# Performance work log

Measured on AMD Instinct MI355X. Metric: run time of the kernel, lower is better.

Reference implementation:

```python
import jax, jax.numpy as jnp
import numpy as np

B, H, I = 4096, 128, 128


def setup_inputs() -> dict:
    key = jax.random.key(0)
    ks = jax.random.split(key, 9)
    # xavier_uniform for W1/W2: fan_in = 2H*2I, fan_out = H*2I (torch treats dim0 as fan_out for >2D differently,
    # but we only need a plausible init; exact init values don't affect correctness of the math)
    def xavier(k, shape):
        fan_in = shape[1] * shape[2] if len(shape) == 3 else shape[0]
        fan_out = shape[0] * shape[2] if len(shape) == 3 else shape[1]
        lim = np.sqrt(6.0 / (fan_in + fan_out))
        return jax.random.uniform(k, shape, jnp.float32, -lim, lim)
    W1 = xavier(ks[0], (H, 2 * H, 2 * I))
    W2 = xavier(ks[1], (H, 2 * H, 2 * I))
    W3 = xavier(ks[2], (2 * H, H))
    fan_in, fan_out = 2 * H * 2 * I, H * 2 * I
    lim = float(np.sqrt(3.0 / (0.5 * (fan_in + fan_out))))
    b1 = jax.random.uniform(ks[3], (H,), jnp.float32, -lim, lim)
    b2 = jax.random.uniform(ks[4], (H,), jnp.float32, -lim, lim)
    in0 = jax.random.normal(ks[5], (B, I), jnp.float32)
    in1 = jax.random.normal(ks[6], (B, I), jnp.float32)
    st0 = jax.random.normal(ks[7], (B, H), jnp.float32)
    st1 = jax.random.normal(ks[8], (B, H), jnp.float32)
    return {"in0": in0, "in1": in1, "st0": st0, "st1": st1,
            "W1": W1, "b1": b1, "W2": W2, "b2": b2, "W3": W3}


def reference(in0, in1, st0, st1, W1, b1, W2, b2, W3):
    s = jnp.concatenate([st0, st1], axis=1)  # [B, 2H]
    x = jnp.concatenate([in0, in1], axis=1)  # [B, 2I]
    # Trilinear contraction; same math as outer-product-then-contract:
    # einsum('ij,ik->ijk') then ('ijk,ljk->il')  ==  'bj,bk,ljk->bl'
    m1 = jnp.einsum('bj,bk,ljk->bl', s, x, W1)  # [B, H]
    m2 = jnp.einsum('bj,bk,ljk->bl', s, x, W2)  # [B, H]
    u = jax.nn.sigmoid(m2 + b2)
    state_tilda = jnp.tanh(m1 + b1)
    new_state = u * state_tilda + (1.0 - u) * (s @ W3)
    return new_state
```

## Files before the change

kernel.cpp:

```cpp
#include <hip/hip_runtime.h>
#include <hip/hip_bf16.h>
#include <stdint.h>


typedef short bf8 __attribute__((ext_vector_type(8)));
typedef float f32x4 __attribute__((ext_vector_type(4)));

static constexpr size_t WT_OFF  = 0;
static constexpr size_t XBF_OFF = 33554432 + 2097152;
static constexpr size_t MP_OFF  = XBF_OFF + 2097152;

__device__ __forceinline__ unsigned f2bf(float f) {
    unsigned u = __builtin_bit_cast(unsigned, f);
    return (u + 0x7fffu + ((u >> 16) & 1u)) >> 16;
}
__device__ __forceinline__ unsigned pack2bf(float a, float b) {
    return f2bf(a) | (f2bf(b) << 16);
}

__global__ void prep_wx(const float* __restrict__ W1, const float* __restrict__ W2,
                        const float* __restrict__ in0, const float* __restrict__ in1,
                        uint4* __restrict__ Wt, unsigned* __restrict__ x_bf) {
    int bx = blockIdx.x;
    if (bx < 8192) {
        const int tid  = threadIdx.x;
        const int lane = tid & 63, wave = tid >> 6;
        const unsigned f = bx * 4 + wave;
        const unsigned n16 = f >> 11;
        const unsigned kchunk = (f >> 1) & 1023u;
        const unsigned kst = f & 1u;
        const unsigned n = n16 * 16 + (lane & 15);
        const unsigned K = kchunk * 64 + kst * 32 + (lane >> 4) * 8;
        const float* src = (n < 128 ? W1 + ((size_t)n << 16)
                                    : W2 + ((size_t)(n - 128) << 16)) + K;
        float4 a = ((const float4*)src)[0];
        float4 b = ((const float4*)src)[1];
        uint4 o;
        o.x = pack2bf(a.x, a.y); o.y = pack2bf(a.z, a.w);
        o.z = pack2bf(b.x, b.y); o.w = pack2bf(b.z, b.w);
        Wt[(size_t)f * 64 + lane] = o;
    } else {
        unsigned v = (bx - 8192) * 256 + threadIdx.x;
        unsigned b = v >> 6;
        unsigned j4 = (v & 63u) * 4u;
        const float* src = (j4 < 128) ? (in0 + (size_t)b * 128 + j4)
                                      : (in1 + (size_t)b * 128 + (j4 - 128));
        float4 a = *(const float4*)src;
        uint2 o;
        o.x = pack2bf(a.x, a.y);
        o.y = pack2bf(a.z, a.w);
        ((uint2*)x_bf)[v] = o;
    }
}

__launch_bounds__(256, 2)
__global__ void gemm_p(const unsigned char* __restrict__ Wt,
                       const float* __restrict__ st0, const float* __restrict__ st1,
                       const __hip_bfloat16* __restrict__ x_bf,
                       float* __restrict__ Mpart) {
    const int bx = blockIdx.x;
    const int ks = bx & 7;
    const int nt = (bx >> 3) & 1;
    const int mt = bx >> 4;
    const int b0 = mt << 7, n0 = nt << 7;
    const int tid  = threadIdx.x;
    const int lane = tid & 63, wave = tid >> 6;
    const int l15 = lane & 15, l4 = lane >> 4;

    __shared__ __align__(16) float Sl[32 * 132];
    for (int idx = tid; idx < 4096; idx += 256) {
        int r = idx >> 5, j = idx & 31;
        int jg = ks * 32 + j;
        float v = (jg < 128) ? st0[(size_t)(b0 + r) * 128 + jg]
                             : st1[(size_t)(b0 + r) * 128 + (jg - 128)];
        Sl[j * 132 + r] = v;
    }
    __syncthreads();

    const int n16_0 = __builtin_amdgcn_readfirstlane(nt * 8 + wave * 2 + 0);
    const int n16_1 = __builtin_amdgcn_readfirstlane(nt * 8 + wave * 2 + 1);
    const unsigned char* wb0 = Wt + ((size_t)n16_0 << 21);
    const unsigned char* wb1 = Wt + ((size_t)n16_1 << 21);

    f32x4 racc[8][2];
    #pragma unroll
    for (int mf = 0; mf < 8; ++mf)
        #pragma unroll
        for (int nf = 0; nf < 2; ++nf)
            racc[mf][nf] = (f32x4){0.f, 0.f, 0.f, 0.f};
    const f32x4 zacc = (f32x4){0.f, 0.f, 0.f, 0.f};

    bf8 a[8][2];
    bf8 buf[2][2][2];

    unsigned vo = (unsigned)lane * 16u + (unsigned)ks * 262144u;

    for (int q = 0; q < 4; ++q) {
        #pragma unroll
        for (int mf = 0; mf < 8; ++mf) {
            const __hip_bfloat16* xp =
                x_bf + (size_t)((b0 + mf * 16 + l15) * 256 + q * 64 + l4 * 8);
            a[mf][0] = *(const bf8*)(xp);
            a[mf][1] = *(const bf8*)(xp + 32);
        }
        buf[0][0][0] = *(const bf8*)(wb0 + vo);
        buf[0][0][1] = *(const bf8*)(wb0 + vo + 1024);
        buf[0][1][0] = *(const bf8*)(wb1 + vo);
        buf[0][1][1] = *(const bf8*)(wb1 + vo + 1024);
        vo += 8192;

        const float* svp = Sl + l4 * 4;

        for (int jb = 0; jb < 4; ++jb) {
            #pragma unroll
            for (int jj = 0; jj < 8; ++jj) {
                const int pp = jj & 1;
                buf[pp ^ 1][0][0] = *(const bf8*)(wb0 + vo);
                buf[pp ^ 1][0][1] = *(const bf8*)(wb0 + vo + 1024);
                buf[pp ^ 1][1][0] = *(const bf8*)(wb1 + vo);
                buf[pp ^ 1][1][1] = *(const bf8*)(wb1 + vo + 1024);
                vo += 8192;
                f32x4 sv[8];
                #pragma unroll
                for (int mf = 0; mf < 8; ++mf)
                    sv[mf] = *(const f32x4*)(svp + mf * 16);
                svp += 132;
                #pragma unroll
                for (int nf = 0; nf < 2; ++nf) {
                    bf8 bf0 = buf[pp][nf][0];
                    bf8 bf1 = buf[pp][nf][1];
                    #pragma unroll
                    for (int mf = 0; mf < 8; ++mf) {
                        f32x4 m0 = __builtin_amdgcn_mfma_f32_16x16x32_bf16(a[mf][0], bf0, zacc, 0, 0, 0);
                        m0 = __builtin_amdgcn_mfma_f32_16x16x32_bf16(a[mf][1], bf1, m0, 0, 0, 0);
                        racc[mf][nf] += sv[mf] * m0;
                    }
                }
            }
        }
        vo += 2048 - 33 * 8192;
    }

    float* mp = Mpart + ((size_t)ks << 20);
    #pragma unroll
    for (int mf = 0; mf < 8; ++mf)
        #pragma unroll
        for (int nf = 0; nf < 2; ++nf) {
            int b = b0 + mf * 16 + l4 * 4;
            int n = n0 + wave * 32 + nf * 16 + l15;
            #pragma unroll
            for (int r = 0; r < 4; ++r)
                mp[(size_t)(b + r) * 256 + n] = racc[mf][nf][r];
        }
}

__global__ void epilogue(const float* __restrict__ st0, const float* __restrict__ st1,
                         const float* __restrict__ b1, const float* __restrict__ b2,
                         const float* __restrict__ W3, const float* __restrict__ Mpart,
                         float* __restrict__ out) {
    const int tid = threadIdx.x;
    const int h = tid & 127, rg = tid >> 7;
    const int bbase = blockIdx.x * 8;
    __shared__ float srow[8][256];
    #pragma unroll
    for (int i = 0; i < 8; ++i) {
        int idx = i * 256 + tid;
        int r = idx >> 8, j = idx & 255;
        float v = (j < 128) ? st0[(size_t)(bbase + r) * 128 + j]
                            : st1[(size_t)(bbase + r) * 128 + (j - 128)];
        srow[r][j] = v;
    }
    __syncthreads();
    float acc0 = 0.f, acc1 = 0.f, acc2 = 0.f, acc3 = 0.f;
    for (int j = 0; j < 256; ++j) {
        float w = W3[j * 128 + h];
        acc0 += srow[rg][j] * w;
        acc1 += srow[rg + 2][j] * w;
        acc2 += srow[rg + 4][j] * w;
        acc3 += srow[rg + 6][j] * w;
    }
    float accs[4] = {acc0, acc1, acc2, acc3};
    float bb1 = b1[h], bb2 = b2[h];
    #pragma unroll
    for (int i = 0; i < 4; ++i) {
        int b = bbase + rg + i * 2;
        float m1 = 0.f, m2 = 0.f;
        #pragma unroll
        for (int k = 0; k < 8; ++k) {
            m1 += Mpart[((size_t)k << 20) + (size_t)b * 256 + h];
            m2 += Mpart[((size_t)k << 20) + (size_t)b * 256 + 128 + h];
        }
        float u = 1.0f / (1.0f + expf(-(m2 + bb2)));
        float t = tanhf(m1 + bb1);
        out[(size_t)b * 128 + h] = u * t + (1.0f - u) * accs[i];
    }
}

extern "C" void kernel_launch(void* const* d_in, const int* in_sizes, int n_in,
                              void* d_out, int out_size, void* d_ws, size_t ws_size,
                              hipStream_t stream) {
    const float* in0 = (const float*)d_in[0];
    const float* in1 = (const float*)d_in[1];
    const float* st0 = (const float*)d_in[2];
    const float* st1 = (const float*)d_in[3];
    const float* W1  = (const float*)d_in[4];
    const float* b1  = (const float*)d_in[5];
    const float* W2  = (const float*)d_in[6];
    const float* b2  = (const float*)d_in[7];
    const float* W3  = (const float*)d_in[8];
    float* out = (float*)d_out;
    char* ws = (char*)d_ws;

    unsigned char* Wt   = (unsigned char*)(ws + WT_OFF);
    unsigned*      x_bf = (unsigned*)(ws + XBF_OFF);
    float*         Mp   = (float*)(ws + MP_OFF);

    prep_wx<<<9216, 256, 0, stream>>>(W1, W2, in0, in1, (uint4*)Wt, x_bf);
    gemm_p<<<512, 256, 0, stream>>>(Wt, st0, st1, (const __hip_bfloat16*)x_bf, Mp);
    epilogue<<<512, 256, 0, stream>>>(st0, st1, b1, b2, W3, Mp, out);
}
```

Baseline: 251.8 us.

## Switch trilinear GEMM to 32x32x16 MFMA tiles with matching weight layout

The weight pre-pack layout is changed to 32-wide n fragments, and the main kernel now uses 32x32x16 bf16 MFMAs, with each wave owning one 32-column slice and four 32-row tiles. Four chained MFMAs cover a 64-wide k chunk before the per-row state scale is applied. The aim is higher MFMA throughput per instruction and fewer weight/x loads per FLOP. It keeps 64 accumulator floats per lane plus operand registers. Separately, the epilogue is split into twice as many blocks of 4 rows, with its inner loop unrolled, for more parallelism.

```diff
diff --git a/kernel.cpp b/kernel.cpp
--- a/kernel.cpp
+++ b/kernel.cpp
@@ -5,6 +5,7 @@
 
 typedef short bf8 __attribute__((ext_vector_type(8)));
 typedef float f32x4 __attribute__((ext_vector_type(4)));
+typedef float f32x16 __attribute__((ext_vector_type(16)));
 
 static constexpr size_t WT_OFF  = 0;
 static constexpr size_t XBF_OFF = 33554432 + 2097152;
@@ -26,11 +27,11 @@
         const int tid  = threadIdx.x;
         const int lane = tid & 63, wave = tid >> 6;
         const unsigned f = bx * 4 + wave;
-        const unsigned n16 = f >> 11;
-        const unsigned kchunk = (f >> 1) & 1023u;
-        const unsigned kst = f & 1u;
-        const unsigned n = n16 * 16 + (lane & 15);
-        const unsigned K = kchunk * 64 + kst * 32 + (lane >> 4) * 8;
+        const unsigned n32 = f >> 12;
+        const unsigned kchunk = (f >> 2) & 1023u;
+        const unsigned ksub = f & 3u;
+        const unsigned n = n32 * 32 + (lane & 31);
+        const unsigned K = kchunk * 64 + ksub * 16 + (lane >> 5) * 8;
         const float* src = (n < 128 ? W1 + ((size_t)n << 16)
                                     : W2 + ((size_t)(n - 128) << 16)) + K;
         float4 a = ((const float4*)src)[0];
@@ -65,7 +66,7 @@
     const int b0 = mt << 7, n0 = nt << 7;
     const int tid  = threadIdx.x;
     const int lane = tid & 63, wave = tid >> 6;
-    const int l15 = lane & 15, l4 = lane >> 4;
+    const int l31 = lane & 31, hi = lane >> 5;
 
     __shared__ __align__(16) float Sl[32 * 132];
     for (int idx = tid; idx < 4096; idx += 256) {
@@ -77,80 +78,75 @@
     }
     __syncthreads();
 
-    const int n16_0 = __builtin_amdgcn_readfirstlane(nt * 8 + wave * 2 + 0);
-    const int n16_1 = __builtin_amdgcn_readfirstlane(nt * 8 + wave * 2 + 1);
-    const unsigned char* wb0 = Wt + ((size_t)n16_0 << 21);
-    const unsigned char* wb1 = Wt + ((size_t)n16_1 << 21);
-
-    f32x4 racc[8][2];
-    #pragma unroll
-    for (int mf = 0; mf < 8; ++mf)
-        #pragma unroll
-        for (int nf = 0; nf < 2; ++nf)
-            racc[mf][nf] = (f32x4){0.f, 0.f, 0.f, 0.f};
-    const f32x4 zacc = (f32x4){0.f, 0.f, 0.f, 0.f};
-
-    bf8 a[8][2];
-    bf8 buf[2][2][2];
-
-    unsigned vo = (unsigned)lane * 16u + (unsigned)ks * 262144u;
+    const int n32 = __builtin_amdgcn_readfirstlane(nt * 4 + wave);
+    const unsigned char* wb = Wt + ((size_t)n32 << 22);
+
+    f32x16 racc[4];
+    #pragma unroll
+    for (int mf = 0; mf < 4; ++mf)
+        #pragma unroll
+        for (int e = 0; e < 16; ++e) racc[mf][e] = 0.f;
+    f32x16 z16;
+    #pragma unroll
+    for (int e = 0; e < 16; ++e) z16[e] = 0.f;
+
+    bf8 a[4][4];
+    bf8 buf[2][4];
+
+    unsigned vo = (unsigned)lane * 16u + (unsigned)ks * 524288u;
 
     for (int q = 0; q < 4; ++q) {
         #pragma unroll
-        for (int mf = 0; mf < 8; ++mf) {
+        for (int mf = 0; mf < 4; ++mf) {
             const __hip_bfloat16* xp =
-                x_bf + (size_t)((b0 + mf * 16 + l15) * 256 + q * 64 + l4 * 8);
-            a[mf][0] = *(const bf8*)(xp);
-            a[mf][1] = *(const bf8*)(xp + 32);
-        }
-        buf[0][0][0] = *(const bf8*)(wb0 + vo);
-        buf[0][0][1] = *(const bf8*)(wb0 + vo + 1024);
-        buf[0][1][0] = *(const bf8*)(wb1 + vo);
-        buf[0][1][1] = *(const bf8*)(wb1 + vo + 1024);
-        vo += 8192;
-
-        const float* svp = Sl + l4 * 4;
-
-        for (int jb = 0; jb < 4; ++jb) {
+                x_bf + (size_t)((b0 + mf * 32 + l31) * 256 + q * 64 + hi * 8);
             #pragma unroll
-            for (int jj = 0; jj < 8; ++jj) {
-                const int pp = jj & 1;
-                buf[pp ^ 1][0][0] = *(const bf8*)(wb0 + vo);
-                buf[pp ^ 1][0][1] = *(const bf8*)(wb0 + vo + 1024);
-                buf[pp ^ 1][1][0] = *(const bf8*)(wb1 + vo);
-                buf[pp ^ 1][1][1] = *(const bf8*)(wb1 + vo + 1024);
-                vo += 8192;
-                f32x4 sv[8];
+            for (int ksub = 0; ksub < 4; ++ksub)
+                a[mf][ksub] = *(const bf8*)(xp + ksub * 16);
+        }
+        #pragma unroll
+        for (int ksub = 0; ksub < 4; ++ksub)
+            buf[0][ksub] = *(const bf8*)(wb + vo + ksub * 1024);
+        vo += 16384;
+
+        const float* svp = Sl + hi * 4;
+
+        for (int jb = 0; jb < 16; ++jb) {
+            #pragma unroll
+            for (int jj = 0; jj < 2; ++jj) {
+                const int pp = jj;
                 #pragma unroll
-                for (int mf = 0; mf < 8; ++mf)
-                    sv[mf] = *(const f32x4*)(svp + mf * 16);
-                svp += 132;
+                for (int ksub = 0; ksub < 4; ++ksub)
+                    buf[pp ^ 1][ksub] = *(const bf8*)(wb + vo + ksub * 1024);
+                vo += 16384;
                 #pragma unroll
-                for (int nf = 0; nf < 2; ++nf) {
-                    bf8 bf0 = buf[pp][nf][0];
-                    bf8 bf1 = buf[pp][nf][1];
+                for (int mf = 0; mf < 4; ++mf) {
+                    f32x16 m0 = __builtin_amdgcn_mfma_f32_32x32x16_bf16(a[mf][0], buf[pp][0], z16, 0, 0, 0);
+                    m0 = __builtin_amdgcn_mfma_f32_32x32x16_bf16(a[mf][1], buf[pp][1], m0, 0, 0, 0);
+                    m0 = __builtin_amdgcn_mfma_f32_32x32x16_bf16(a[mf][2], buf[pp][2], m0, 0, 0, 0);
+                    m0 = __builtin_amdgcn_mfma_f32_32x32x16_bf16(a[mf][3], buf[pp][3], m0, 0, 0, 0);
                     #pragma unroll
-                    for (int mf = 0; mf < 8; ++mf) {
-                        f32x4 m0 = __builtin_amdgcn_mfma_f32_16x16x32_bf16(a[mf][0], bf0, zacc, 0, 0, 0);
-                        m0 = __builtin_amdgcn_mfma_f32_16x16x32_bf16(a[mf][1], bf1, m0, 0, 0, 0);
-                        racc[mf][nf] += sv[mf] * m0;
+                    for (int g = 0; g < 4; ++g) {
+                        f32x4 sg = *(const f32x4*)(svp + mf * 32 + g * 8);
+                        #pragma unroll
+                        for (int t = 0; t < 4; ++t)
+                            racc[mf][g * 4 + t] += sg[t] * m0[g * 4 + t];
                     }
                 }
+                svp += 132;
             }
         }
-        vo += 2048 - 33 * 8192;
+        vo += 4096 - 33 * 16384;
     }
 
     float* mp = Mpart + ((size_t)ks << 20);
-    #pragma unroll
-    for (int mf = 0; mf < 8; ++mf)
-        #pragma unroll
-        for (int nf = 0; nf < 2; ++nf) {
-            int b = b0 + mf * 16 + l4 * 4;
-            int n = n0 + wave * 32 + nf * 16 + l15;
-            #pragma unroll
-            for (int r = 0; r < 4; ++r)
-                mp[(size_t)(b + r) * 256 + n] = racc[mf][nf][r];
+    const int n = n0 + (n32 & 3) * 32 + l31;
+    #pragma unroll
+    for (int mf = 0; mf < 4; ++mf)
+        #pragma unroll
+        for (int r = 0; r < 16; ++r) {
+            int row = b0 + mf * 32 + (r & 3) + 8 * (r >> 2) + 4 * hi;
+            mp[(size_t)row * 256 + n] = racc[mf][r];
         }
 }
 
@@ -160,10 +156,10 @@
                          float* __restrict__ out) {
     const int tid = threadIdx.x;
     const int h = tid & 127, rg = tid >> 7;
-    const int bbase = blockIdx.x * 8;
-    __shared__ float srow[8][256];
-    #pragma unroll
-    for (int i = 0; i < 8; ++i) {
+    const int bbase = blockIdx.x * 4;
+    __shared__ float srow[4][256];
+    #pragma unroll
+    for (int i = 0; i < 4; ++i) {
         int idx = i * 256 + tid;
         int r = idx >> 8, j = idx & 255;
         float v = (j < 128) ? st0[(size_t)(bbase + r) * 128 + j]
@@ -171,18 +167,17 @@
         srow[r][j] = v;
     }
     __syncthreads();
-    float acc0 = 0.f, acc1 = 0.f, acc2 = 0.f, acc3 = 0.f;
+    float acc0 = 0.f, acc1 = 0.f;
+    #pragma unroll 8
     for (int j = 0; j < 256; ++j) {
         float w = W3[j * 128 + h];
         acc0 += srow[rg][j] * w;
         acc1 += srow[rg + 2][j] * w;
-        acc2 += srow[rg + 4][j] * w;
-        acc3 += srow[rg + 6][j] * w;
-    }
-    float accs[4] = {acc0, acc1, acc2, acc3};
+    }
+    float accs[2] = {acc0, acc1};
     float bb1 = b1[h], bb2 = b2[h];
     #pragma unroll
-    for (int i = 0; i < 4; ++i) {
+    for (int i = 0; i < 2; ++i) {
         int b = bbase + rg + i * 2;
         float m1 = 0.f, m2 = 0.f;
         #pragma unroll
@@ -217,5 +212,5 @@
 
     prep_wx<<<9216, 256, 0, stream>>>(W1, W2, in0, in1, (uint4*)Wt, x_bf);
     gemm_p<<<512, 256, 0, stream>>>(Wt, st0, st1, (const __hip_bfloat16*)x_bf, Mp);
-    epilogue<<<512, 256, 0, stream>>>(st0, st1, b1, b2, W3, Mp, out);
-}
+    epilogue<<<1024, 256, 0, stream>>>(st0, st1, b1, b2, W3, Mp, out);
+}
```

Measured after the change: 326.9 us. 29.8% more time.

## Reorder packed weight layout for sequential streaming, deepen prefetch, split epilogue finer

Applied to the files above, without the earlier changes.

The bf16 weight repack now orders fragments in the exact sequence each GEMM block consumes them (split, q, j, kst). Each wave then streams weights contiguously with a fixed 2 KB stride. The register prefetch ring grows from 2 to 4 stages, with three stages preloaded before the main loop, to hide more global-load latency. The epilogue handles 4 rows per block across 1024 blocks instead of 8 rows across 512, with an unrolled W3 loop, to raise parallelism. The deeper ring costs more VGPRs, which could strain the 2-blocks-per-CU launch bound.

```diff
diff --git a/kernel.cpp b/kernel.cpp
--- a/kernel.cpp
+++ b/kernel.cpp
@@ -27,8 +27,13 @@
         const int lane = tid & 63, wave = tid >> 6;
         const unsigned f = bx * 4 + wave;
         const unsigned n16 = f >> 11;
-        const unsigned kchunk = (f >> 1) & 1023u;
-        const unsigned kst = f & 1u;
+        const unsigned r2  = f & 2047u;
+        const unsigned ks  = r2 >> 8;
+        const unsigned rem = r2 & 255u;
+        const unsigned q   = rem >> 6;
+        const unsigned jl  = (rem >> 1) & 31u;
+        const unsigned kst = rem & 1u;
+        const unsigned kchunk = (ks * 32 + jl) * 4 + q;
         const unsigned n = n16 * 16 + (lane & 15);
         const unsigned K = kchunk * 64 + kst * 32 + (lane >> 4) * 8;
         const float* src = (n < 128 ? W1 + ((size_t)n << 16)
@@ -91,9 +96,18 @@
     const f32x4 zacc = (f32x4){0.f, 0.f, 0.f, 0.f};
 
     bf8 a[8][2];
-    bf8 buf[2][2][2];
+    bf8 buf[4][2][2];
 
     unsigned vo = (unsigned)lane * 16u + (unsigned)ks * 262144u;
+
+    #pragma unroll
+    for (int w = 0; w < 3; ++w) {
+        buf[w][0][0] = *(const bf8*)(wb0 + vo);
+        buf[w][0][1] = *(const bf8*)(wb0 + vo + 1024);
+        buf[w][1][0] = *(const bf8*)(wb1 + vo);
+        buf[w][1][1] = *(const bf8*)(wb1 + vo + 1024);
+        vo += 2048;
+    }
 
     for (int q = 0; q < 4; ++q) {
         #pragma unroll
@@ -103,23 +117,20 @@
             a[mf][0] = *(const bf8*)(xp);
             a[mf][1] = *(const bf8*)(xp + 32);
         }
-        buf[0][0][0] = *(const bf8*)(wb0 + vo);
-        buf[0][0][1] = *(const bf8*)(wb0 + vo + 1024);
-        buf[0][1][0] = *(const bf8*)(wb1 + vo);
-        buf[0][1][1] = *(const bf8*)(wb1 + vo + 1024);
-        vo += 8192;
 
         const float* svp = Sl + l4 * 4;
 
-        for (int jb = 0; jb < 4; ++jb) {
+        for (int jb = 0; jb < 8; ++jb) {
             #pragma unroll
-            for (int jj = 0; jj < 8; ++jj) {
-                const int pp = jj & 1;
-                buf[pp ^ 1][0][0] = *(const bf8*)(wb0 + vo);
-                buf[pp ^ 1][0][1] = *(const bf8*)(wb0 + vo + 1024);
-                buf[pp ^ 1][1][0] = *(const bf8*)(wb1 + vo);
-                buf[pp ^ 1][1][1] = *(const bf8*)(wb1 + vo + 1024);
-                vo += 8192;
+            for (int jj = 0; jj < 4; ++jj) {
+                {
+                    const int ps = (jj + 3) & 3;
+                    buf[ps][0][0] = *(const bf8*)(wb0 + vo);
+                    buf[ps][0][1] = *(const bf8*)(wb0 + vo + 1024);
+                    buf[ps][1][0] = *(const bf8*)(wb1 + vo);
+                    buf[ps][1][1] = *(const bf8*)(wb1 + vo + 1024);
+                    vo += 2048;
+                }
                 f32x4 sv[8];
                 #pragma unroll
                 for (int mf = 0; mf < 8; ++mf)
@@ -127,8 +138,8 @@
                 svp += 132;
                 #pragma unroll
                 for (int nf = 0; nf < 2; ++nf) {
-                    bf8 bf0 = buf[pp][nf][0];
-                    bf8 bf1 = buf[pp][nf][1];
+                    bf8 bf0 = buf[jj][nf][0];
+                    bf8 bf1 = buf[jj][nf][1];
                     #pragma unroll
                     for (int mf = 0; mf < 8; ++mf) {
                         f32x4 m0 = __builtin_amdgcn_mfma_f32_16x16x32_bf16(a[mf][0], bf0, zacc, 0, 0, 0);
@@ -138,7 +149,6 @@
                 }
             }
         }
-        vo += 2048 - 33 * 8192;
     }
 
     float* mp = Mpart + ((size_t)ks << 20);
@@ -160,10 +170,10 @@
                          float* __restrict__ out) {
     const int tid = threadIdx.x;
     const int h = tid & 127, rg = tid >> 7;
-    const int bbase = blockIdx.x * 8;
-    __shared__ float srow[8][256];
-    #pragma unroll
-    for (int i = 0; i < 8; ++i) {
+    const int bbase = blockIdx.x * 4;
+    __shared__ float srow[4][256];
+    #pragma unroll
+    for (int i = 0; i < 4; ++i) {
         int idx = i * 256 + tid;
         int r = idx >> 8, j = idx & 255;
         float v = (j < 128) ? st0[(size_t)(bbase + r) * 128 + j]
@@ -171,18 +181,17 @@
         srow[r][j] = v;
     }
     __syncthreads();
-    float acc0 = 0.f, acc1 = 0.f, acc2 = 0.f, acc3 = 0.f;
+    float acc0 = 0.f, acc1 = 0.f;
+    #pragma unroll 8
     for (int j = 0; j < 256; ++j) {
         float w = W3[j * 128 + h];
         acc0 += srow[rg][j] * w;
         acc1 += srow[rg + 2][j] * w;
-        acc2 += srow[rg + 4][j] * w;
-        acc3 += srow[rg + 6][j] * w;
-    }
-    float accs[4] = {acc0, acc1, acc2, acc3};
+    }
+    float accs[2] = {acc0, acc1};
     float bb1 = b1[h], bb2 = b2[h];
     #pragma unroll
-    for (int i = 0; i < 4; ++i) {
+    for (int i = 0; i < 2; ++i) {
         int b = bbase + rg + i * 2;
         float m1 = 0.f, m2 = 0.f;
         #pragma unroll
@@ -217,5 +226,5 @@
 
     prep_wx<<<9216, 256, 0, stream>>>(W1, W2, in0, in1, (uint4*)Wt, x_bf);
     gemm_p<<<512, 256, 0, stream>>>(Wt, st0, st1, (const __hip_bfloat16*)x_bf, Mp);
-    epilogue<<<512, 256, 0, stream>>>(st0, st1, b1, b2, W3, Mp, out);
-}
+    epilogue<<<1024, 256, 0, stream>>>(st0, st1, b1, b2, W3, Mp, out);
+}
```

After: 383.4 us. 1.52x slower.
